# Kernel tuning notes

Measured on AMD Instinct MI355X. Metric: run time of the kernel, lower is better.

## Reference

```python
import jax, jax.numpy as jnp
import numpy as np

H = 4          # num_heads
D = 256        # hidden_dim
HD = D // H    # head_dim = 64
EPS = 1e-5


def setup_inputs() -> dict:
    key = jax.random.key(0)
    ks = jax.random.split(key, 12)
    B, S = 2, 4096
    sc = 1.0 / np.sqrt(D)
    return {
        "query": jax.random.normal(ks[0], (B, S, D), jnp.float32),
        "key_": jax.random.normal(ks[1], (B, S, D), jnp.float32),
        "value": jax.random.normal(ks[2], (B, S, D), jnp.float32),
        "wq": jax.random.normal(ks[3], (D, D), jnp.float32) * sc,
        "bq": jax.random.normal(ks[4], (D,), jnp.float32) * 0.01,
        "wk": jax.random.normal(ks[5], (D, D), jnp.float32) * sc,
        "bk": jax.random.normal(ks[6], (D,), jnp.float32) * 0.01,
        "wv": jax.random.normal(ks[7], (D, D), jnp.float32) * sc,
        "bv": jax.random.normal(ks[8], (D,), jnp.float32) * 0.01,
        "wo": jax.random.normal(ks[9], (D, D), jnp.float32) * sc,
        "bo": jax.random.normal(ks[10], (D,), jnp.float32) * 0.01,
        "gamma": jnp.ones((D,), jnp.float32),
        "beta": jnp.zeros((D,), jnp.float32),
    }


def reference(query, key_, value, wq, bq, wk, bk, wv, bv, wo, bo, gamma, beta):
    B, S, _ = query.shape
    # Linear projections (torch Linear: x @ W.T + b), split into heads -> [B,H,S,HD]
    q = (query @ wq.T + bq).reshape(B, S, H, HD).transpose(0, 2, 1, 3)
    k = (key_ @ wk.T + bk).reshape(B, S, H, HD).transpose(0, 2, 1, 3)
    v = (value @ wv.T + bv).reshape(B, S, H, HD).transpose(0, 2, 1, 3)
    scale = 1.0 / jnp.sqrt(jnp.array(HD, query.dtype))
    scores = jnp.einsum('bhqd,bhkd->bhqk', q, k) * scale  # [B,H,S,S]
    attn = jax.nn.softmax(scores, axis=-1)
    out = jnp.einsum('bhqk,bhkd->bhqd', attn, v)          # [B,H,S,HD]
    out = out.transpose(0, 2, 1, 3).reshape(B, S, D)
    out = out @ wo.T + bo
    # LayerNorm(eps=1e-5)
    mu = out.mean(-1, keepdims=True)
    var = ((out - mu) ** 2).mean(-1, keepdims=True)
    return (out - mu) * jax.lax.rsqrt(var + EPS) * gamma + beta
```

## Files before the change

kernel.cpp:

```cpp
#include <hip/hip_runtime.h>
#include <hip/hip_bf16.h>

using bf16 = __hip_bfloat16;
typedef __attribute__((ext_vector_type(8))) short bf16x8;
typedef __attribute__((ext_vector_type(4))) short short4v;
typedef __attribute__((ext_vector_type(4))) float f32x4;

#define MFMA(a, b, c) __builtin_amdgcn_mfma_f32_16x16x32_bf16((a), (b), (c), 0, 0, 0)

#define S_LEN 4096
#define D_MODEL 256
#define NH 4
#define HD 64
#define NTOK 8192
#define PROW 72
#define XROW 264
#define SM_SHIFT 16.0f


static __device__ __forceinline__ short f2bf(float f) {
  bf16 h = __float2bfloat16(f);
  return *reinterpret_cast<short*>(&h);
}

static __device__ __forceinline__ void stage1k(const bf16* g, short* l, int lane) {
  const int ri = lane >> 3;
  const int ci = lane & 7;
  const bf16* gp = g + ri * 64 + ((ci ^ ri) << 3);
  __builtin_amdgcn_global_load_lds(
      (const __attribute__((address_space(1))) void*)gp,
      (__attribute__((address_space(3))) void*)l, 16, 0, 0);
}

__global__ __launch_bounds__(256) void pack_w(
    const float* __restrict__ wq, const float* __restrict__ wk,
    const float* __restrict__ wv, const float* __restrict__ wo,
    bf16* __restrict__ wpk) {
  const int mat = blockIdx.x >> 4;
  const int nt  = blockIdx.x & 15;
  const float* W = (mat == 0) ? wq : (mat == 1) ? wk : (mat == 2) ? wv : wo;
  bf16* dst = wpk + ((size_t)(mat * 16 + nt)) * 4096;
#pragma unroll
  for (int it = 0; it < 16; ++it) {
    const int idx = it * 256 + threadIdx.x;
    const int kkt = idx >> 9;
    const int rem = idx & 511;
    const int L = rem >> 3, j = rem & 7;
    const int row = nt * 16 + (L & 15);
    const int col = kkt * 32 + (L >> 4) * 8 + j;
    dst[kkt * 512 + rem] = __float2bfloat16(W[(size_t)row * D_MODEL + col]);
  }
}

__global__ __launch_bounds__(256) void qkv_proj(
    const float* __restrict__ q_in, const float* __restrict__ k_in, const float* __restrict__ v_in,
    const float* __restrict__ bq_, const float* __restrict__ bk_, const float* __restrict__ bv_,
    const bf16* __restrict__ wpk,
    bf16* __restrict__ qg, bf16* __restrict__ kg, bf16* __restrict__ vtg) {
  const int tid  = threadIdx.x;
  const int wave = tid >> 6;
  const int lane = tid & 63;
  const int quad = lane >> 4;
  const int l16  = lane & 15;
  const int z  = blockIdx.y;
  const int m0 = blockIdx.x * 64;

  const float* X  = (z == 0) ? q_in : (z == 1) ? k_in : v_in;
  const float* Bp = (z == 0) ? bq_  : (z == 1) ? bk_  : bv_;
  const bf16* wp = wpk + (size_t)z * 65536;

  __shared__ short xs[64 * XROW];

#pragma unroll
  for (int it = 0; it < 16; ++it) {
    const int idx = it * 256 + tid;
    const int row = idx >> 6;
    const int c4  = idx & 63;
    const float4 f = *(const float4*)(X + (size_t)(m0 + row) * D_MODEL + c4 * 4);
    short4v s;
    s[0] = f2bf(f.x); s[1] = f2bf(f.y); s[2] = f2bf(f.z); s[3] = f2bf(f.w);
    *(short4v*)&xs[row * XROW + c4 * 4] = s;
  }
  __syncthreads();

  f32x4 acc[4][4] = {};

  if (z < 2) {
    for (int kki = 0; kki < 8; ++kki) {
      const int kk = kki * 32;
      bf16x8 bfr[4];
#pragma unroll
      for (int nt = 0; nt < 4; ++nt)
        bfr[nt] = *(const bf16x8*)(wp + ((wave * 4 + nt) * 8 + kki) * 512 + lane * 8);
#pragma unroll
      for (int ms = 0; ms < 4; ++ms) {
        bf16x8 a = *(const bf16x8*)&xs[(ms * 16 + l16) * XROW + kk + quad * 8];
#pragma unroll
        for (int nt = 0; nt < 4; ++nt) acc[ms][nt] = MFMA(a, bfr[nt], acc[ms][nt]);
      }
    }
    bf16* dst = (z == 0) ? qg : kg;
    const float scale = (z == 0) ? 0.125f : 1.0f;
    const int h = wave;
#pragma unroll
    for (int nt = 0; nt < 4; ++nt) {
      const int o = wave * 64 + nt * 16 + l16;
      const float bias = Bp[o];
      const int hd = o & 63;
#pragma unroll
      for (int ms = 0; ms < 4; ++ms)
#pragma unroll
        for (int r = 0; r < 4; ++r) {
          const int t = m0 + ms * 16 + quad * 4 + r;
          const int b_ = t >> 12, s = t & 4095;
          dst[((size_t)((b_ * NH + h) * S_LEN + s)) * HD + hd] =
              __float2bfloat16((acc[ms][nt][r] + bias) * scale);
        }
    }
  } else {
    for (int kki = 0; kki < 8; ++kki) {
      const int kk = kki * 32;
      bf16x8 bx[4];
#pragma unroll
      for (int ts = 0; ts < 4; ++ts)
        bx[ts] = *(const bf16x8*)&xs[(ts * 16 + l16) * XROW + kk + quad * 8];
#pragma unroll
      for (int ot = 0; ot < 4; ++ot) {
        bf16x8 aw = *(const bf16x8*)(wp + ((wave * 4 + ot) * 8 + kki) * 512 + lane * 8);
#pragma unroll
        for (int ts = 0; ts < 4; ++ts) acc[ot][ts] = MFMA(aw, bx[ts], acc[ot][ts]);
      }
    }
    const int h = wave;
    const int b_ = m0 >> 12;
    const int jt = (m0 & 4095) >> 6;
#pragma unroll
    for (int ot = 0; ot < 4; ++ot)
#pragma unroll
      for (int r = 0; r < 4; ++r) {
        const int o = wave * 64 + ot * 16 + quad * 4 + r;
        const float bias = Bp[o];
        const int hd = o & 63;
        bf16* vrow = vtg + (((size_t)((b_ * NH + h) * (S_LEN / 64) + jt)) * HD + hd) * 64;
#pragma unroll
        for (int ts = 0; ts < 4; ++ts)
          vrow[ts * 16 + l16] = __float2bfloat16(acc[ot][ts][r] + bias);
      }
  }
}

__global__ __launch_bounds__(256) void attn_fwd(
    const bf16* qg, const bf16* kg, const bf16* vtg, bf16* attn) {
  const int wave = threadIdx.x >> 6;
  const int lane = threadIdx.x & 63;
  const int quad = lane >> 4;
  const int l16  = lane & 15;
  const int bh = blockIdx.x & 7;
  const int q0 = (blockIdx.x >> 3) * 128;

  const bf16* qb = qg  + (size_t)bh * S_LEN * HD;
  const bf16* kb = kg  + (size_t)bh * S_LEN * HD;
  const bf16* vb = vtg + (size_t)bh * S_LEN * HD;

  __shared__ short kbuf[2][2 * 4096];
  __shared__ short vbuf[2][2 * 4096];
  __shared__ short p_lds[4 * 16 * PROW];

  bf16x8 qf[2][2];
#pragma unroll
  for (int qs = 0; qs < 2; ++qs) {
    const bf16* qrow = qb + (size_t)(q0 + wave * 32 + qs * 16 + l16) * HD;
    qf[qs][0] = *(const bf16x8*)(qrow + quad * 8);
    qf[qs][1] = *(const bf16x8*)(qrow + 32 + quad * 8);
  }

  float l_acc[2] = {0.f, 0.f};
  f32x4 oT[2][4] = {};
  const int pb = wave * (16 * PROW) + l16 * PROW;
  const int sw = l16 & 7;
  const int c0 = wave * 2;

#define STAGE_ROUND(b, r)                                                   \
  {                                                                         \
    _Pragma("unroll")                                                       \
    for (int sub = 0; sub < 2; ++sub) {                                     \
      const bf16* kt = kb + (size_t)(2 * (r) + sub) * 4096;                 \
      const bf16* vt_ = vb + (size_t)(2 * (r) + sub) * 4096;                \
      _Pragma("unroll")                                                     \
      for (int q = 0; q < 2; ++q) {                                         \
        stage1k(kt + (c0 + q) * 512, &kbuf[b][sub * 4096 + (c0 + q) * 512], lane); \
        stage1k(vt_ + (c0 + q) * 512, &vbuf[b][sub * 4096 + (c0 + q) * 512], lane); \
      }                                                                     \
    }                                                                       \
  }

  STAGE_ROUND(0, 0)

  for (int t = 0; t < 32; ++t) {
    const int buf = t & 1;
    __syncthreads();
    if (t + 1 < 32) STAGE_ROUND(buf ^ 1, t + 1)

#pragma unroll
    for (int sub = 0; sub < 2; ++sub) {
      const short* kB = &kbuf[buf][sub * 4096];
      const short* vB = &vbuf[buf][sub * 4096];

      bf16x8 kf[4][2];
#pragma unroll
      for (int ct = 0; ct < 4; ++ct) {
        const int rbase = (ct * 16 + l16) * 64;
        kf[ct][0] = *(const bf16x8*)&kB[rbase + ((quad ^ sw) << 3)];
        kf[ct][1] = *(const bf16x8*)&kB[rbase + (((quad + 4) ^ sw) << 3)];
      }

      f32x4 st[2][4] = {};
#pragma unroll
      for (int qs = 0; qs < 2; ++qs)
#pragma unroll
        for (int ct = 0; ct < 4; ++ct) {
          st[qs][ct] = MFMA(kf[ct][0], qf[qs][0], st[qs][ct]);
          st[qs][ct] = MFMA(kf[ct][1], qf[qs][1], st[qs][ct]);
        }

      bf16x8 vf[4][2];
#pragma unroll
      for (int tt = 0; tt < 4; ++tt) {
        const int rbase = (tt * 16 + l16) * 64;
        vf[tt][0] = *(const bf16x8*)&vB[rbase + ((quad ^ sw) << 3)];
        vf[tt][1] = *(const bf16x8*)&vB[rbase + (((quad + 4) ^ sw) << 3)];
      }

#pragma unroll
      for (int qs = 0; qs < 2; ++qs) {
#pragma unroll
        for (int ct = 0; ct < 4; ++ct)
#pragma unroll
          for (int r = 0; r < 4; ++r) {
            const float p = __expf(st[qs][ct][r] - SM_SHIFT);
            st[qs][ct][r] = p;
            l_acc[qs] += p;
          }

        asm volatile("" ::: "memory");
#pragma unroll
        for (int ct = 0; ct < 4; ++ct) {
          short4v pk;
          pk[0] = f2bf(st[qs][ct][0]);
          pk[1] = f2bf(st[qs][ct][1]);
          pk[2] = f2bf(st[qs][ct][2]);
          pk[3] = f2bf(st[qs][ct][3]);
          *(short4v*)&p_lds[pb + ct * 16 + quad * 4] = pk;
        }
        asm volatile("" ::: "memory");
        bf16x8 bp0 = *(const bf16x8*)&p_lds[pb + quad * 8];
        bf16x8 bp1 = *(const bf16x8*)&p_lds[pb + 32 + quad * 8];

#pragma unroll
        for (int tt = 0; tt < 4; ++tt) {
          oT[qs][tt] = MFMA(vf[tt][0], bp0, oT[qs][tt]);
          oT[qs][tt] = MFMA(vf[tt][1], bp1, oT[qs][tt]);
        }
      }
    }
  }
#undef STAGE_ROUND

  const int b_ = bh >> 2, h = bh & 3;
#pragma unroll
  for (int qs = 0; qs < 2; ++qs) {
    float l = l_acc[qs];
    l += __shfl_xor(l, 16);
    l += __shfl_xor(l, 32);
    const float inv = 1.0f / l;
    bf16* ob = attn + ((size_t)(b_ * S_LEN + q0 + wave * 32 + qs * 16 + l16)) * D_MODEL + h * HD;
#pragma unroll
    for (int t = 0; t < 4; ++t) {
      short4v pk;
#pragma unroll
      for (int r = 0; r < 4; ++r) pk[r] = f2bf(oT[qs][t][r] * inv);
      *(short4v*)(ob + t * 16 + quad * 4) = pk;
    }
  }
}

__global__ __launch_bounds__(256) void out_ln(
    const bf16* __restrict__ attn, const bf16* __restrict__ wpk,
    const float* __restrict__ bo_, const float* __restrict__ gamma,
    const float* __restrict__ beta, float* __restrict__ out) {
  const int tid = threadIdx.x;
  const int wave = tid >> 6;
  const int lane = tid & 63;
  const int quad = lane >> 4;
  const int l16  = lane & 15;
  const int t0 = blockIdx.x * 16;
  const bf16* wp = wpk + (size_t)3 * 65536;

  __shared__ short as_[16 * XROW];
  __shared__ float ybuf[16 * 256];
  __shared__ float mu_s[16], rs_s[16];

#pragma unroll
  for (int it = 0; it < 2; ++it) {
    const int idx = it * 256 + tid;
    const int row = idx >> 5;
    const int c8  = idx & 31;
    bf16x8 v = *(const bf16x8*)(attn + (size_t)(t0 + row) * D_MODEL + c8 * 8);
    *(bf16x8*)&as_[row * XROW + c8 * 8] = v;
  }
  __syncthreads();

  f32x4 acc[4] = {};
  for (int kki = 0; kki < 8; ++kki) {
    const int kk = kki * 32;
    bf16x8 a = *(const bf16x8*)&as_[l16 * XROW + kk + quad * 8];
#pragma unroll
    for (int nt = 0; nt < 4; ++nt) {
      bf16x8 b = *(const bf16x8*)(wp + ((wave * 4 + nt) * 8 + kki) * 512 + lane * 8);
      acc[nt] = MFMA(a, b, acc[nt]);
    }
  }
#pragma unroll
  for (int nt = 0; nt < 4; ++nt) {
    const int o = wave * 64 + nt * 16 + l16;
    const float bias = bo_[o];
#pragma unroll
    for (int r = 0; r < 4; ++r) ybuf[(quad * 4 + r) * 256 + o] = acc[nt][r] + bias;
  }
  __syncthreads();

#pragma unroll
  for (int rr = 0; rr < 4; ++rr) {
    const int row = wave * 4 + rr;
    float s1 = 0.f, s2 = 0.f;
#pragma unroll
    for (int c = 0; c < 4; ++c) {
      const float v = ybuf[row * 256 + c * 64 + lane];
      s1 += v;
      s2 += v * v;
    }
#pragma unroll
    for (int m = 32; m >= 1; m >>= 1) {
      s1 += __shfl_xor(s1, m);
      s2 += __shfl_xor(s2, m);
    }
    if (lane == 0) {
      const float mu = s1 * (1.f / 256.f);
      const float var = s2 * (1.f / 256.f) - mu * mu;
      mu_s[row] = mu;
      rs_s[row] = rsqrtf(var + 1e-5f);
    }
  }
  __syncthreads();

  const float g  = gamma[tid];
  const float be = beta[tid];
#pragma unroll 4
  for (int row = 0; row < 16; ++row) {
    const float v = ybuf[row * 256 + tid];
    const float o = (v - mu_s[row]) * rs_s[row] * g + be;
    out[(size_t)(t0 + row) * D_MODEL + tid] = o;
  }
}

extern "C" void kernel_launch(void* const* d_in, const int* in_sizes, int n_in,
                              void* d_out, int out_size, void* d_ws, size_t ws_size,
                              hipStream_t stream) {
  const float* q_in  = (const float*)d_in[0];
  const float* k_in  = (const float*)d_in[1];
  const float* v_in  = (const float*)d_in[2];
  const float* wq    = (const float*)d_in[3];
  const float* bq    = (const float*)d_in[4];
  const float* wk    = (const float*)d_in[5];
  const float* bk    = (const float*)d_in[6];
  const float* wv    = (const float*)d_in[7];
  const float* bv    = (const float*)d_in[8];
  const float* wo    = (const float*)d_in[9];
  const float* bo    = (const float*)d_in[10];
  const float* gamma = (const float*)d_in[11];
  const float* beta  = (const float*)d_in[12];
  float* out = (float*)d_out;

  const size_t SEG = (size_t)NTOK * D_MODEL;
  bf16* qg   = (bf16*)d_out;
  bf16* kg   = (bf16*)d_out + SEG;
  bf16* vtt  = (bf16*)d_ws;
  bf16* attn = (bf16*)d_ws + SEG;
  bf16* wpk  = (bf16*)d_ws + 2 * SEG;

  pack_w<<<dim3(64), 256, 0, stream>>>(wq, wk, wv, wo, wpk);
  qkv_proj<<<dim3(128, 3), 256, 0, stream>>>(q_in, k_in, v_in, bq, bk, bv, wpk,
                                             qg, kg, vtt);
  attn_fwd<<<dim3(256), 256, 0, stream>>>(qg, kg, vtt, attn);
  out_ln<<<dim3(512), 256, 0, stream>>>(attn, wpk, bo, gamma, beta, out);
}
```

Baseline: 187.4 us.

## Split attention key range across two blocks and coalesce projection stores via LDS

```diff
diff --git a/kernel.cpp b/kernel.cpp
--- a/kernel.cpp
+++ b/kernel.cpp
@@ -15,12 +15,18 @@
 #define NTOK 8192
 #define PROW 72
 #define XROW 264
+#define TROWV 72
 #define SM_SHIFT 16.0f
 
 
 static __device__ __forceinline__ short f2bf(float f) {
   bf16 h = __float2bfloat16(f);
   return *reinterpret_cast<short*>(&h);
+}
+
+static __device__ __forceinline__ float bf2f(short s) {
+  const unsigned int u = ((unsigned int)(unsigned short)s) << 16;
+  return __builtin_bit_cast(float, u);
 }
 
 static __device__ __forceinline__ void stage1k(const bf16* g, short* l, int lane) {
@@ -70,6 +76,7 @@
   const bf16* wp = wpk + (size_t)z * 65536;
 
   __shared__ short xs[64 * XROW];
+  __shared__ short tbuf[256 * TROWV];
 
 #pragma unroll
   for (int it = 0; it < 16; ++it) {
@@ -101,21 +108,27 @@
     }
     bf16* dst = (z == 0) ? qg : kg;
     const float scale = (z == 0) ? 0.125f : 1.0f;
-    const int h = wave;
 #pragma unroll
     for (int nt = 0; nt < 4; ++nt) {
       const int o = wave * 64 + nt * 16 + l16;
       const float bias = Bp[o];
-      const int hd = o & 63;
 #pragma unroll
       for (int ms = 0; ms < 4; ++ms)
 #pragma unroll
-        for (int r = 0; r < 4; ++r) {
-          const int t = m0 + ms * 16 + quad * 4 + r;
-          const int b_ = t >> 12, s = t & 4095;
-          dst[((size_t)((b_ * NH + h) * S_LEN + s)) * HD + hd] =
-              __float2bfloat16((acc[ms][nt][r] + bias) * scale);
-        }
+        for (int r = 0; r < 4; ++r)
+          tbuf[(ms * 16 + quad * 4 + r) * XROW + o] =
+              f2bf((acc[ms][nt][r] + bias) * scale);
+    }
+    asm volatile("" ::: "memory");
+    const int h = wave;
+    const int b_ = m0 >> 12, s0 = m0 & 4095;
+    bf16* base = dst + ((size_t)(b_ * NH + h) * S_LEN + s0) * HD;
+#pragma unroll
+    for (int it = 0; it < 8; ++it) {
+      const int s  = it * 8 + (lane >> 3);
+      const int ch = (lane & 7) * 8;
+      bf16x8 v = *(const bf16x8*)&tbuf[s * XROW + h * 64 + ch];
+      *(bf16x8*)(base + (size_t)s * HD + ch) = v;
     }
   } else {
     for (int kki = 0; kki < 8; ++kki) {
@@ -131,32 +144,41 @@
         for (int ts = 0; ts < 4; ++ts) acc[ot][ts] = MFMA(aw, bx[ts], acc[ot][ts]);
       }
     }
+#pragma unroll
+    for (int ot = 0; ot < 4; ++ot)
+#pragma unroll
+      for (int r = 0; r < 4; ++r) {
+        const int o = wave * 64 + ot * 16 + quad * 4 + r;
+        const float bias = Bp[o];
+#pragma unroll
+        for (int ts = 0; ts < 4; ++ts)
+          tbuf[o * TROWV + ts * 16 + l16] = f2bf(acc[ot][ts][r] + bias);
+      }
+    asm volatile("" ::: "memory");
     const int h = wave;
     const int b_ = m0 >> 12;
     const int jt = (m0 & 4095) >> 6;
-#pragma unroll
-    for (int ot = 0; ot < 4; ++ot)
-#pragma unroll
-      for (int r = 0; r < 4; ++r) {
-        const int o = wave * 64 + ot * 16 + quad * 4 + r;
-        const float bias = Bp[o];
-        const int hd = o & 63;
-        bf16* vrow = vtg + (((size_t)((b_ * NH + h) * (S_LEN / 64) + jt)) * HD + hd) * 64;
-#pragma unroll
-        for (int ts = 0; ts < 4; ++ts)
-          vrow[ts * 16 + l16] = __float2bfloat16(acc[ot][ts][r] + bias);
-      }
+    bf16* vbase = vtg + ((size_t)((b_ * NH + h) * (S_LEN / 64) + jt)) * HD * 64;
+#pragma unroll
+    for (int it = 0; it < 8; ++it) {
+      const int hd = it * 8 + (lane >> 3);
+      const int jj = (lane & 7) * 8;
+      bf16x8 v = *(const bf16x8*)&tbuf[(h * 64 + hd) * TROWV + jj];
+      *(bf16x8*)(vbase + (size_t)hd * 64 + jj) = v;
+    }
   }
 }
 
 __global__ __launch_bounds__(256) void attn_fwd(
-    const bf16* qg, const bf16* kg, const bf16* vtg, bf16* attn) {
+    const bf16* qg, const bf16* kg, const bf16* vtg,
+    bf16* part0, bf16* part1, float* lbuf) {
   const int wave = threadIdx.x >> 6;
   const int lane = threadIdx.x & 63;
   const int quad = lane >> 4;
   const int l16  = lane & 15;
-  const int bh = blockIdx.x & 7;
-  const int q0 = (blockIdx.x >> 3) * 128;
+  const int bh   = blockIdx.x & 7;
+  const int half = (blockIdx.x >> 3) & 1;
+  const int q0   = (blockIdx.x >> 4) * 128;
 
   const bf16* qb = qg  + (size_t)bh * S_LEN * HD;
   const bf16* kb = kg  + (size_t)bh * S_LEN * HD;
@@ -194,12 +216,13 @@
     }                                                                       \
   }
 
-  STAGE_ROUND(0, 0)
-
-  for (int t = 0; t < 32; ++t) {
+  const int t0 = half * 16, t1 = t0 + 16;
+  STAGE_ROUND(0, t0)
+
+  for (int t = t0; t < t1; ++t) {
     const int buf = t & 1;
     __syncthreads();
-    if (t + 1 < 32) STAGE_ROUND(buf ^ 1, t + 1)
+    if (t + 1 < t1) STAGE_ROUND(buf ^ 1, t + 1)
 
 #pragma unroll
     for (int sub = 0; sub < 2; ++sub) {
@@ -266,21 +289,49 @@
   }
 #undef STAGE_ROUND
 
+  bf16* part = half ? part1 : part0;
   const int b_ = bh >> 2, h = bh & 3;
 #pragma unroll
   for (int qs = 0; qs < 2; ++qs) {
     float l = l_acc[qs];
     l += __shfl_xor(l, 16);
     l += __shfl_xor(l, 32);
-    const float inv = 1.0f / l;
-    bf16* ob = attn + ((size_t)(b_ * S_LEN + q0 + wave * 32 + qs * 16 + l16)) * D_MODEL + h * HD;
+    const int srow = q0 + wave * 32 + qs * 16 + l16;
+    if (quad == 0)
+      lbuf[half * 32768 + bh * 4096 + srow] = l;
+    bf16* ob = part + ((size_t)(b_ * S_LEN + srow)) * D_MODEL + h * HD;
 #pragma unroll
     for (int t = 0; t < 4; ++t) {
       short4v pk;
 #pragma unroll
-      for (int r = 0; r < 4; ++r) pk[r] = f2bf(oT[qs][t][r] * inv);
+      for (int r = 0; r < 4; ++r) pk[r] = f2bf(oT[qs][t][r]);
       *(short4v*)(ob + t * 16 + quad * 4) = pk;
     }
+  }
+}
+
+__global__ __launch_bounds__(256) void attn_combine(
+    bf16* part0, const bf16* __restrict__ part1, const float* __restrict__ lbuf) {
+  const int tid = threadIdx.x;
+  const int t0 = blockIdx.x * 16;
+#pragma unroll
+  for (int it = 0; it < 2; ++it) {
+    const int c = it * 256 + tid;
+    const int row = c >> 5;
+    const int c8  = c & 31;
+    const int token = t0 + row;
+    const int h = c8 >> 3;
+    const int bh = (token >> 12) * NH + h;
+    const int s = token & 4095;
+    const float li = 1.0f / (lbuf[bh * 4096 + s] + lbuf[32768 + bh * 4096 + s]);
+    const size_t idx = (size_t)token * D_MODEL + c8 * 8;
+    bf16x8 a = *(const bf16x8*)(part0 + idx);
+    bf16x8 b = *(const bf16x8*)(part1 + idx);
+    bf16x8 o;
+#pragma unroll
+    for (int j = 0; j < 8; ++j)
+      o[j] = f2bf((bf2f(a[j]) + bf2f(b[j])) * li);
+    *(bf16x8*)(part0 + idx) = o;
   }
 }
 
@@ -382,15 +433,18 @@
   float* out = (float*)d_out;
 
   const size_t SEG = (size_t)NTOK * D_MODEL;
-  bf16* qg   = (bf16*)d_out;
-  bf16* kg   = (bf16*)d_out + SEG;
-  bf16* vtt  = (bf16*)d_ws;
-  bf16* attn = (bf16*)d_ws + SEG;
-  bf16* wpk  = (bf16*)d_ws + 2 * SEG;
+  bf16* qg    = (bf16*)d_out;
+  bf16* kg    = (bf16*)d_out + SEG;
+  bf16* vtt   = (bf16*)d_ws;
+  bf16* part0 = (bf16*)d_ws + SEG;
+  bf16* part1 = (bf16*)d_ws + 2 * SEG;
+  bf16* wpk   = (bf16*)d_ws + 3 * SEG;
+  float* lbuf = (float*)((bf16*)d_ws + 3 * SEG + 262144);
 
   pack_w<<<dim3(64), 256, 0, stream>>>(wq, wk, wv, wo, wpk);
   qkv_proj<<<dim3(128, 3), 256, 0, stream>>>(q_in, k_in, v_in, bq, bk, bv, wpk,
                                              qg, kg, vtt);
-  attn_fwd<<<dim3(256), 256, 0, stream>>>(qg, kg, vtt, attn);
-  out_ln<<<dim3(512), 256, 0, stream>>>(attn, wpk, bo, gamma, beta, out);
-}
+  attn_fwd<<<dim3(512), 256, 0, stream>>>(qg, kg, vtt, part0, part1, lbuf);
+  attn_combine<<<dim3(512), 256, 0, stream>>>(part0, part1, lbuf);
+  out_ln<<<dim3(512), 256, 0, stream>>>(part0, wpk, bo, gamma, beta, out);
+}
```

After: 169.2 us. 9.7% less time.
